# Kernel tuning notes

Measured on AMD Instinct MI355X. Metric: run time of the kernel, lower is better.

Reference implementation:

```python
import jax, jax.numpy as jnp
import numpy as np

N = 20000      # nodes
E = 640000     # edges
FIN = 256
FQK = 256


def setup_inputs() -> dict:
    key = jax.random.key(0)
    kx, ks, kd, kw = jax.random.split(key, 4)
    x = jax.random.normal(kx, (N, FIN), dtype=jnp.float32)
    # src must be sorted (original scatter_softmax assumes grouped index);
    # force last element to N-1 so nbatches == N as in batch[-1]+1.
    src = jnp.sort(jax.random.randint(ks, (E,), 0, N))
    src = src.at[-1].set(N - 1)
    dest = jax.random.randint(kd, (E,), 0, N)
    ei = jnp.stack([src, dest]).astype(jnp.int64)
    # nn.Linear(Fin, 2*Fqk, bias=False) weight: [2*Fqk, Fin]
    bound = 1.0 / np.sqrt(FIN)
    W = jax.random.uniform(kw, (2 * FQK, FIN), dtype=jnp.float32,
                           minval=-bound, maxval=bound)
    return {"x": x, "ei": ei, "W": W}


def reference(x, ei, W):
    src, dest = ei[0], ei[1]
    n_nodes = x.shape[0]
    scaling = FQK ** -0.5
    qk = x @ W.T                      # [N, 2*Fqk]
    q, k = jnp.split(qk, 2, axis=-1)  # each [N, Fqk]
    q = q * scaling
    # per-edge dot product: (q[src] . k[dest])  -> [E]
    aw = jnp.einsum('ef,ef->e', q[src], k[dest])
    # scatter softmax over edges grouped by src node (raw exp, as original)
    ex = jnp.exp(aw)
    expsum = jax.ops.segment_sum(ex, src, num_segments=n_nodes)  # [N]
    return ex / expsum[src]
```

## Files before the change

kernel.cpp:

```cpp
#include <hip/hip_runtime.h>
#include <cmath>

#define FIN 256
#define FQK 256
#define SCALING 0.0625f
#define MAX_SEG 256

typedef __bf16 bf16_t;
typedef bf16_t bf16x8 __attribute__((ext_vector_type(8)));
typedef float  f32x4  __attribute__((ext_vector_type(4)));

__device__ __forceinline__ unsigned short f2bf(float f) {
    unsigned int u = __float_as_uint(f);
    u += 0x7FFFu + ((u >> 16) & 1u);
    return (unsigned short)(u >> 16);
}
__device__ __forceinline__ float bf_lo(unsigned int w) { return __uint_as_float(w << 16); }
__device__ __forceinline__ float bf_hi(unsigned int w) { return __uint_as_float(w & 0xFFFF0000u); }

#define ASTRIDE 40
#define GROWS   32

__global__ __launch_bounds__(256) void gemm_qk_kernel(const float* __restrict__ x,
                                                      const float* __restrict__ W,
                                                      unsigned short* __restrict__ qarr,
                                                      unsigned short* __restrict__ karr,
                                                      int N) {
    __shared__ unsigned short sA[GROWS * ASTRIDE];

    const int h    = blockIdx.y;
    const float* __restrict__ Wh = W + (size_t)h * FQK * FIN;
    unsigned short* __restrict__ outp = h ? karr : qarr;
    const float scale = h ? 1.0f : SCALING;

    const int t    = threadIdx.x;
    const int wv   = t >> 6;
    const int lane = t & 63;
    const int q    = lane >> 4;
    const int m16  = lane & 15;
    const int n0   = blockIdx.x * GROWS;
    const int f0   = wv * 64;

    f32x4 acc[2][4] = {};

    const int srow = t >> 3;
    const int skc  = (t & 7) * 4;

    for (int kc = 0; kc < FIN; kc += 32) {
        {
            const int n = n0 + srow;
            float4 v = make_float4(0.f, 0.f, 0.f, 0.f);
            if (n < N) v = *(const float4*)(x + (size_t)n * FIN + kc + skc);
            unsigned short* p = &sA[srow * ASTRIDE + skc];
            p[0] = f2bf(v.x); p[1] = f2bf(v.y); p[2] = f2bf(v.z); p[3] = f2bf(v.w);
        }
        __syncthreads();

        bf16x8 afrag[2];
#pragma unroll
        for (int mt = 0; mt < 2; ++mt)
            afrag[mt] = *(const bf16x8*)&sA[(mt * 16 + m16) * ASTRIDE + q * 8];
#pragma unroll
        for (int ft = 0; ft < 4; ++ft) {
            const int f = f0 + ft * 16 + m16;
            const float4 b0 = *(const float4*)(Wh + (size_t)f * FIN + kc + q * 8);
            const float4 b1 = *(const float4*)(Wh + (size_t)f * FIN + kc + q * 8 + 4);
            union { unsigned short s[8]; bf16x8 v; } bu;
            bu.s[0] = f2bf(b0.x); bu.s[1] = f2bf(b0.y); bu.s[2] = f2bf(b0.z); bu.s[3] = f2bf(b0.w);
            bu.s[4] = f2bf(b1.x); bu.s[5] = f2bf(b1.y); bu.s[6] = f2bf(b1.z); bu.s[7] = f2bf(b1.w);
#pragma unroll
            for (int mt = 0; mt < 2; ++mt)
                acc[mt][ft] = __builtin_amdgcn_mfma_f32_16x16x32_bf16(afrag[mt], bu.v,
                                                                     acc[mt][ft], 0, 0, 0);
        }
        __syncthreads();
    }

#pragma unroll
    for (int mt = 0; mt < 2; ++mt) {
#pragma unroll
        for (int r = 0; r < 4; ++r) {
            const int n = n0 + mt * 16 + q * 4 + r;
            if (n < N) {
#pragma unroll
                for (int ft = 0; ft < 4; ++ft)
                    outp[(size_t)n * FIN + f0 + ft * 16 + m16] = f2bf(acc[mt][ft][r] * scale);
            }
        }
    }
}

__global__ __launch_bounds__(256) void seg_kernel(const int* __restrict__ src,
                                                  int* __restrict__ seg, int N, int E) {
    const int n = blockIdx.x * 256 + threadIdx.x;
    if (n > N) return;
    int lo = 0, hi = E;
    while (lo < hi) {
        const int mid = (lo + hi) >> 1;
        if (src[mid] < n) lo = mid + 1; else hi = mid;
    }
    seg[n] = lo;
}

__global__ __launch_bounds__(256) void node_edge_kernel(const unsigned short* __restrict__ qarr,
                                                        const unsigned short* __restrict__ karr,
                                                        const int* __restrict__ dest,
                                                        const int* __restrict__ seg,
                                                        float* __restrict__ out, int N) {
    __shared__ float exlds[4][MAX_SEG];

    const int w    = threadIdx.x >> 6;
    const int lane = threadIdx.x & 63;
    const int n    = blockIdx.x * 4 + w;
    const int g    = lane >> 4;
    const int j    = lane & 15;

    int   s0 = 0, cnt = 0;
    float inv = 0.f;

    if (n < N) {
        s0 = seg[n];
        cnt = seg[n + 1] - s0;
    }

    if (cnt > 0) {
        const uint4* __restrict__ qr = (const uint4*)(qarr + (size_t)n * FIN);
        const uint4 qa0 = qr[j];
        const uint4 qa1 = qr[16 + j];
        float4 xa, xb, xc, xd;
        xa.x = bf_lo(qa0.x); xa.y = bf_hi(qa0.x); xa.z = bf_lo(qa0.y); xa.w = bf_hi(qa0.y);
        xb.x = bf_lo(qa0.z); xb.y = bf_hi(qa0.z); xb.z = bf_lo(qa0.w); xb.w = bf_hi(qa0.w);
        xc.x = bf_lo(qa1.x); xc.y = bf_hi(qa1.x); xc.z = bf_lo(qa1.y); xc.w = bf_hi(qa1.y);
        xd.x = bf_lo(qa1.z); xd.y = bf_hi(qa1.z); xd.z = bf_lo(qa1.w); xd.w = bf_hi(qa1.w);

        float sum = 0.f;
        for (int base = 0; base < cnt; base += 64) {
            const int m = min(64, cnt - base);
            const int vd = (lane < m) ? dest[s0 + base + lane] : 0;
            const int nit = (m + 3) >> 2;
            for (int it = 0; it < nit; it += 2) {
                const int  eg0 = it * 4 + g;
                const int  eg1 = eg0 + 4;
                const bool v0  = eg0 < m;
                const bool v1  = eg1 < m;
                const int  d0  = __shfl(vd, eg0, 64);
                const int  d1  = __shfl(vd, eg1, 64);
                const uint4* __restrict__ kr0 = (const uint4*)(karr + (size_t)(v0 ? d0 : 0) * FIN);
                const uint4* __restrict__ kr1 = (const uint4*)(karr + (size_t)(v1 ? d1 : 0) * FIN);
                const uint4 q00 = kr0[j];
                const uint4 q01 = kr0[16 + j];
                const uint4 q10 = kr1[j];
                const uint4 q11 = kr1[16 + j];

                float a0 = 0.f, a1 = 0.f;
                a0 += bf_lo(q00.x) * xa.x + bf_hi(q00.x) * xa.y
                    + bf_lo(q00.y) * xa.z + bf_hi(q00.y) * xa.w
                    + bf_lo(q00.z) * xb.x + bf_hi(q00.z) * xb.y
                    + bf_lo(q00.w) * xb.z + bf_hi(q00.w) * xb.w;
                a0 += bf_lo(q01.x) * xc.x + bf_hi(q01.x) * xc.y
                    + bf_lo(q01.y) * xc.z + bf_hi(q01.y) * xc.w
                    + bf_lo(q01.z) * xd.x + bf_hi(q01.z) * xd.y
                    + bf_lo(q01.w) * xd.z + bf_hi(q01.w) * xd.w;
                a1 += bf_lo(q10.x) * xa.x + bf_hi(q10.x) * xa.y
                    + bf_lo(q10.y) * xa.z + bf_hi(q10.y) * xa.w
                    + bf_lo(q10.z) * xb.x + bf_hi(q10.z) * xb.y
                    + bf_lo(q10.w) * xb.z + bf_hi(q10.w) * xb.w;
                a1 += bf_lo(q11.x) * xc.x + bf_hi(q11.x) * xc.y
                    + bf_lo(q11.y) * xc.z + bf_hi(q11.y) * xc.w
                    + bf_lo(q11.z) * xd.x + bf_hi(q11.z) * xd.y
                    + bf_lo(q11.w) * xd.z + bf_hi(q11.w) * xd.w;

                a0 += __shfl_xor(a0, 1, 64);
                a1 += __shfl_xor(a1, 1, 64);
                a0 += __shfl_xor(a0, 2, 64);
                a1 += __shfl_xor(a1, 2, 64);
                a0 += __shfl_xor(a0, 4, 64);
                a1 += __shfl_xor(a1, 4, 64);
                a0 += __shfl_xor(a0, 8, 64);
                a1 += __shfl_xor(a1, 8, 64);

                if (v0) {
                    const float ex = __expf(a0);
                    sum += ex;
                    const int idx = base + eg0;
                    if (j == 0 && idx < MAX_SEG) exlds[w][idx] = ex;
                }
                if (v1) {
                    const float ex = __expf(a1);
                    sum += ex;
                    const int idx = base + eg1;
                    if (j == 0 && idx < MAX_SEG) exlds[w][idx] = ex;
                }
            }
        }
        sum += __shfl_xor(sum, 16, 64);
        sum += __shfl_xor(sum, 32, 64);
        inv = 1.0f / sum;
    }

    __syncthreads();

    if (cnt > 0) {
        const int lim = cnt < MAX_SEG ? cnt : MAX_SEG;
        for (int i = lane; i < lim; i += 64)
            out[s0 + i] = exlds[w][i] * inv;
    }
}

extern "C" void kernel_launch(void* const* d_in, const int* in_sizes, int n_in,
                              void* d_out, int out_size, void* d_ws, size_t ws_size,
                              hipStream_t stream) {
    const float* x  = (const float*)d_in[0];
    const int*   ei = (const int*)d_in[1];
    const float* W  = (const float*)d_in[2];
    float* out = (float*)d_out;

    const int N = in_sizes[0] / FIN;
    const int E = in_sizes[1] / 2;

    unsigned short* qarr = (unsigned short*)d_ws;
    unsigned short* karr = qarr + (size_t)N * FIN;
    int*            seg  = (int*)(karr + (size_t)N * FIN);

    dim3 ggrid((N + GROWS - 1) / GROWS, 2);
    gemm_qk_kernel<<<ggrid, 256, 0, stream>>>(x, W, qarr, karr, N);

    seg_kernel<<<(N + 256) / 256, 256, 0, stream>>>(ei, seg, N, E);

    node_edge_kernel<<<(N + 3) / 4, 256, 0, stream>>>(qarr, karr, ei + E, seg, out, N);
}
```

Baseline: 152.1 us.

## Pre-convert W to bf16 and hold B fragments in registers in QK GEMM

A new prep kernel converts W to packed bf16 once per call. The GEMM then loads each wave's whole B slice into registers up front and stages the full 32x256 x tile in LDS with a single barrier, replacing the per-k-chunk load/convert/sync loop. This removes repeated fp32 W loads and conversions and seven barrier pairs per block. In exchange it adds an extra launch, 128 VGPRs of B fragments that may reduce occupancy, and about 17 KB of LDS per block.

```diff
diff --git a/kernel.cpp b/kernel.cpp
--- a/kernel.cpp
+++ b/kernel.cpp
@@ -17,19 +17,32 @@
 }
 __device__ __forceinline__ float bf_lo(unsigned int w) { return __uint_as_float(w << 16); }
 __device__ __forceinline__ float bf_hi(unsigned int w) { return __uint_as_float(w & 0xFFFF0000u); }
-
-#define ASTRIDE 40
-#define GROWS   32
+__device__ __forceinline__ unsigned int pack2(float a, float b) {
+    return (unsigned int)f2bf(a) | ((unsigned int)f2bf(b) << 16);
+}
+
+__global__ __launch_bounds__(256) void prep_wb_kernel(const float* __restrict__ W,
+                                                      unsigned int* __restrict__ Wb2) {
+    const int i = blockIdx.x * 256 + threadIdx.x;
+    const float4 v = *(const float4*)(W + (size_t)i * 4);
+    uint2 p;
+    p.x = pack2(v.x, v.y);
+    p.y = pack2(v.z, v.w);
+    *(uint2*)(Wb2 + (size_t)i * 2) = p;
+}
+
+#define GROWS    32
+#define SAROW    264
 
 __global__ __launch_bounds__(256) void gemm_qk_kernel(const float* __restrict__ x,
-                                                      const float* __restrict__ W,
+                                                      const unsigned short* __restrict__ Wb,
                                                       unsigned short* __restrict__ qarr,
                                                       unsigned short* __restrict__ karr,
                                                       int N) {
-    __shared__ unsigned short sA[GROWS * ASTRIDE];
+    __shared__ unsigned short sA[GROWS * SAROW];
 
     const int h    = blockIdx.y;
-    const float* __restrict__ Wh = W + (size_t)h * FQK * FIN;
+    const unsigned short* __restrict__ Wbh = Wb + (size_t)h * FQK * FIN;
     unsigned short* __restrict__ outp = h ? karr : qarr;
     const float scale = h ? 1.0f : SCALING;
 
@@ -41,39 +54,48 @@
     const int n0   = blockIdx.x * GROWS;
     const int f0   = wv * 64;
 
+    uint4 bfrag[4][8];
+#pragma unroll
+    for (int ft = 0; ft < 4; ++ft) {
+        const unsigned short* __restrict__ brow = Wbh + (size_t)(f0 + ft * 16 + m16) * FIN;
+#pragma unroll
+        for (int kc = 0; kc < 8; ++kc)
+            bfrag[ft][kc] = *(const uint4*)(brow + kc * 32 + q * 8);
+    }
+
+    {
+        const int r  = t >> 6;
+        const int c4 = (t & 63) * 4;
+#pragma unroll
+        for (int u = 0; u < 8; ++u) {
+            const int row = u * 4 + r;
+            const int n = n0 + row;
+            float4 v = make_float4(0.f, 0.f, 0.f, 0.f);
+            if (n < N) v = *(const float4*)(x + (size_t)n * FIN + c4);
+            uint2 p;
+            p.x = pack2(v.x, v.y);
+            p.y = pack2(v.z, v.w);
+            *(uint2*)&sA[row * SAROW + c4] = p;
+        }
+    }
+    __syncthreads();
+
     f32x4 acc[2][4] = {};
-
-    const int srow = t >> 3;
-    const int skc  = (t & 7) * 4;
-
-    for (int kc = 0; kc < FIN; kc += 32) {
-        {
-            const int n = n0 + srow;
-            float4 v = make_float4(0.f, 0.f, 0.f, 0.f);
-            if (n < N) v = *(const float4*)(x + (size_t)n * FIN + kc + skc);
-            unsigned short* p = &sA[srow * ASTRIDE + skc];
-            p[0] = f2bf(v.x); p[1] = f2bf(v.y); p[2] = f2bf(v.z); p[3] = f2bf(v.w);
-        }
-        __syncthreads();
-
+#pragma unroll
+    for (int kc = 0; kc < 8; ++kc) {
         bf16x8 afrag[2];
 #pragma unroll
         for (int mt = 0; mt < 2; ++mt)
-            afrag[mt] = *(const bf16x8*)&sA[(mt * 16 + m16) * ASTRIDE + q * 8];
+            afrag[mt] = *(const bf16x8*)&sA[(mt * 16 + m16) * SAROW + kc * 32 + q * 8];
 #pragma unroll
         for (int ft = 0; ft < 4; ++ft) {
-            const int f = f0 + ft * 16 + m16;
-            const float4 b0 = *(const float4*)(Wh + (size_t)f * FIN + kc + q * 8);
-            const float4 b1 = *(const float4*)(Wh + (size_t)f * FIN + kc + q * 8 + 4);
-            union { unsigned short s[8]; bf16x8 v; } bu;
-            bu.s[0] = f2bf(b0.x); bu.s[1] = f2bf(b0.y); bu.s[2] = f2bf(b0.z); bu.s[3] = f2bf(b0.w);
-            bu.s[4] = f2bf(b1.x); bu.s[5] = f2bf(b1.y); bu.s[6] = f2bf(b1.z); bu.s[7] = f2bf(b1.w);
+            union { uint4 u; bf16x8 v; } bu;
+            bu.u = bfrag[ft][kc];
 #pragma unroll
             for (int mt = 0; mt < 2; ++mt)
                 acc[mt][ft] = __builtin_amdgcn_mfma_f32_16x16x32_bf16(afrag[mt], bu.v,
                                                                      acc[mt][ft], 0, 0, 0);
         }
-        __syncthreads();
     }
 
 #pragma unroll
@@ -220,10 +242,13 @@
 
     unsigned short* qarr = (unsigned short*)d_ws;
     unsigned short* karr = qarr + (size_t)N * FIN;
-    int*            seg  = (int*)(karr + (size_t)N * FIN);
+    unsigned short* Wb   = karr + (size_t)N * FIN;
+    int*            seg  = (int*)(Wb + (size_t)2 * FQK * FIN);
+
+    prep_wb_kernel<<<(2 * FQK * FIN) / (256 * 4), 256, 0, stream>>>(W, (unsigned int*)Wb);
 
     dim3 ggrid((N + GROWS - 1) / GROWS, 2);
-    gemm_qk_kernel<<<ggrid, 256, 0, stream>>>(x, W, qarr, karr, N);
+    gemm_qk_kernel<<<ggrid, 256, 0, stream>>>(x, Wb, qarr, karr, N);
 
     seg_kernel<<<(N + 256) / 256, 256, 0, stream>>>(ei, seg, N, E);
 
```

New measurement: 140.6 us. 1.08x faster.
